# Performance work log

Hardware: AMD Instinct MI355X
Metric: run time of the kernel (lower is better)

## Reference

```python
import jax, jax.numpy as jnp
import numpy as np

MARGIN = 1.0


def setup_inputs() -> dict:
    key = jax.random.key(0)
    k1, k2, k3 = jax.random.split(key, 3)
    N, F = 4096, 512
    a = jax.random.normal(k1, (N, F), dtype=jnp.float32)
    b = jax.random.normal(k2, (N, F), dtype=jnp.float32)
    labels = jax.random.randint(k3, (N,), 0, 16, dtype=jnp.int32)
    return {"a": a, "b": b, "labels": labels}


def reference(a, b, labels):
    # D[i, j] = ||b_i - a_j||  (torch: Xa=a[None], Xb=b[:,None], sum over feat)
    # GEMM form of the pairwise sqdist; clamp tiny fp negatives before sqrt.
    Dsq = (jnp.sum(b * b, axis=1)[:, None]
           + jnp.sum(a * a, axis=1)[None, :]
           - 2.0 * (b @ a.T))
    D = jnp.sqrt(jnp.maximum(Dsq, 0.0))            # [N, N]
    Dexpm = jnp.exp(MARGIN - D)                    # [N, N]

    same = labels[:, None] == labels[None, :]      # [N, N]
    eye = jnp.eye(labels.shape[0], dtype=bool)
    pos_mask = same & ~eye                         # ordered positive pairs (i, j)
    neg_mask = ~same                               # negative pairs (labels differ)

    # neg_i sum for row i: sum_k Dexpm[i, k] over k with labels[k] != labels[i]
    row_negsum = jnp.sum(jnp.where(neg_mask, Dexpm, 0.0), axis=1)  # [N]

    # J_ij = log(neg_ik_sum + neg_jl_sum) + D[i, j]; hinged and squared
    J = jnp.log(row_negsum[:, None] + row_negsum[None, :]) + D
    hinge_sq = jnp.square(jnp.maximum(J, 0.0))

    num_pos = jnp.sum(pos_mask)
    return jnp.sum(jnp.where(pos_mask, hinge_sq, 0.0)) / (2.0 * num_pos)
```

## Files before the change

kernel.cpp:

```cpp
#include <hip/hip_runtime.h>
#include <math.h>

#define NROW 4096
#define FDIM 512
#define MARGIN 1.0f

typedef __attribute__((ext_vector_type(8))) short short8;
typedef __attribute__((ext_vector_type(4))) float floatx4;

__device__ inline unsigned short f2bf(float x) {
    unsigned u = __float_as_uint(x);
    return (unsigned short)((u + 0x7FFFu + ((u >> 16) & 1u)) >> 16);
}
__device__ inline float h2f(unsigned short u) {
    _Float16 h; __builtin_memcpy(&h, &u, 2); return (float)h;
}
__device__ inline unsigned short f2h(float f) {
    _Float16 h = (_Float16)f; unsigned short u; __builtin_memcpy(&u, &h, 2); return u;
}

__global__ __launch_bounds__(64) void prep_kernel(
    const float* __restrict__ a, const float* __restrict__ b,
    unsigned short* __restrict__ abf, unsigned short* __restrict__ bbf,
    float* __restrict__ na, float* __restrict__ nb,
    float* __restrict__ rns, float* __restrict__ loss) {
    int row  = blockIdx.x;
    int lane = threadIdx.x;
    const float4* a4 = (const float4*)(a + (size_t)row * FDIM);
    const float4* b4 = (const float4*)(b + (size_t)row * FDIM);
    ushort4* au = (ushort4*)(abf + (size_t)row * FDIM);
    ushort4* bu = (ushort4*)(bbf + (size_t)row * FDIM);
    float sa = 0.f, sb = 0.f;
    #pragma unroll
    for (int f = lane; f < FDIM / 4; f += 64) {
        float4 va = a4[f];
        float4 vb = b4[f];
        sa += va.x * va.x + va.y * va.y + va.z * va.z + va.w * va.w;
        sb += vb.x * vb.x + vb.y * vb.y + vb.z * vb.z + vb.w * vb.w;
        ushort4 ua = { f2bf(va.x), f2bf(va.y), f2bf(va.z), f2bf(va.w) };
        ushort4 ub = { f2bf(vb.x), f2bf(vb.y), f2bf(vb.z), f2bf(vb.w) };
        au[f] = ua;
        bu[f] = ub;
    }
    #pragma unroll
    for (int o = 32; o > 0; o >>= 1) {
        sa += __shfl_down(sa, o);
        sb += __shfl_down(sb, o);
    }
    if (lane == 0) {
        na[row] = sa;
        nb[row] = sb;
        rns[row] = 0.f;
        if (row == 0) loss[0] = 0.f;
    }
}

template <int MODE>
__global__ __launch_bounds__(256) void pass_mfma(
    const unsigned short* __restrict__ abf, const unsigned short* __restrict__ bbf,
    const int* __restrict__ labels,
    const float* __restrict__ na, const float* __restrict__ nb,
    float* __restrict__ rns, unsigned short* __restrict__ Dws,
    float* __restrict__ loss_sum)
{
    __shared__ __align__(16) unsigned short smem[17408];
    unsigned short* As0 = smem;
    unsigned short* As1 = smem + 4096;
    unsigned short* Bs0 = smem + 8192;
    unsigned short* Bs1 = smem + 12288;
    __shared__ int   li_s[128], lj_s[128];
    __shared__ float nb_s[128], na_s[128], rbi_s[128], rbj_s[128];

    const int t    = threadIdx.x;
    const int lane = t & 63;
    const int w    = t >> 6;
    const int wi   = w >> 1, wj = w & 1;
    const int bid  = blockIdx.x;
    const int sup  = bid >> 6, loc = bid & 63;
    const int by   = ((sup >> 2) << 3) | (loc >> 3);
    const int bx   = ((sup & 3) << 3) | (loc & 7);
    const int ti   = by * 128;
    const int tj   = bx * 128;
    const int lr   = lane & 15;
    const int lq   = lane >> 4;

    floatx4 acc[4][4];
    #pragma unroll
    for (int i = 0; i < 4; ++i)
        #pragma unroll
        for (int j = 0; j < 4; ++j)
            acc[i][j] = (floatx4){0.f, 0.f, 0.f, 0.f};

    if (t < 128) {
        li_s[t] = labels[ti + t];
        nb_s[t] = nb[ti + t];
        if (MODE == 2) rbi_s[t] = rns[ti + t];
    } else {
        int u = t - 128;
        lj_s[u] = labels[tj + u];
        na_s[u] = na[tj + u];
        if (MODE == 2) rbj_s[u] = rns[tj + u];
    }

    for (int kk = 0; kk < FDIM; kk += 64) {
        #pragma unroll
        for (int l = 0; l < 2; ++l) {
            int c   = t + l * 256;
            int row = c >> 2;
            int q   = c & 3;
            size_t ga = (size_t)(tj + row) * FDIM + kk + q * 8;
            size_t gb = (size_t)(ti + row) * FDIM + kk + q * 8;
            __builtin_amdgcn_global_load_lds(
                (const __attribute__((address_space(1))) unsigned int*)(abf + ga),
                (__attribute__((address_space(3))) unsigned int*)(As0 + c * 8), 16, 0, 0);
            __builtin_amdgcn_global_load_lds(
                (const __attribute__((address_space(1))) unsigned int*)(abf + ga + 32),
                (__attribute__((address_space(3))) unsigned int*)(As1 + c * 8), 16, 0, 0);
            __builtin_amdgcn_global_load_lds(
                (const __attribute__((address_space(1))) unsigned int*)(bbf + gb),
                (__attribute__((address_space(3))) unsigned int*)(Bs0 + c * 8), 16, 0, 0);
            __builtin_amdgcn_global_load_lds(
                (const __attribute__((address_space(1))) unsigned int*)(bbf + gb + 32),
                (__attribute__((address_space(3))) unsigned int*)(Bs1 + c * 8), 16, 0, 0);
        }
        __syncthreads();

        {
            short8 af[4], bf[4];
            #pragma unroll
            for (int ri = 0; ri < 4; ++ri)
                af[ri] = *(const short8*)&Bs0[(wi * 64 + ri * 16 + lr) * 32 + lq * 8];
            #pragma unroll
            for (int rj = 0; rj < 4; ++rj)
                bf[rj] = *(const short8*)&As0[(wj * 64 + rj * 16 + lr) * 32 + lq * 8];
            #pragma unroll
            for (int ri = 0; ri < 4; ++ri)
                #pragma unroll
                for (int rj = 0; rj < 4; ++rj)
                    acc[ri][rj] = __builtin_amdgcn_mfma_f32_16x16x32_bf16(
                        af[ri], bf[rj], acc[ri][rj], 0, 0, 0);
        }
        {
            short8 af[4], bf[4];
            #pragma unroll
            for (int ri = 0; ri < 4; ++ri)
                af[ri] = *(const short8*)&Bs1[(wi * 64 + ri * 16 + lr) * 32 + lq * 8];
            #pragma unroll
            for (int rj = 0; rj < 4; ++rj)
                bf[rj] = *(const short8*)&As1[(wj * 64 + rj * 16 + lr) * 32 + lq * 8];
            #pragma unroll
            for (int ri = 0; ri < 4; ++ri)
                #pragma unroll
                for (int rj = 0; rj < 4; ++rj)
                    acc[ri][rj] = __builtin_amdgcn_mfma_f32_16x16x32_bf16(
                        af[ri], bf[rj], acc[ri][rj], 0, 0, 0);
        }
        __syncthreads();
    }

    if (MODE == 0 || MODE == 1) {
        unsigned short* D_s = smem;
        #pragma unroll
        for (int ri = 0; ri < 4; ++ri) {
            float rs[4] = {0.f, 0.f, 0.f, 0.f};
            #pragma unroll
            for (int rj = 0; rj < 4; ++rj) {
                int   jl  = wj * 64 + rj * 16 + lr;
                float naj = na_s[jl];
                int   ljv = lj_s[jl];
                #pragma unroll
                for (int r = 0; r < 4; ++r) {
                    int   il  = wi * 64 + ri * 16 + lq * 4 + r;
                    float dsq = nb_s[il] + naj - 2.f * acc[ri][rj][r];
                    float D   = sqrtf(fmaxf(dsq, 0.f));
                    if (li_s[il] != ljv) rs[r] += __expf(MARGIN - D);
                    if (MODE == 0) D_s[il * 136 + jl] = f2h(D);
                }
            }
            #pragma unroll
            for (int r = 0; r < 4; ++r) {
                #pragma unroll
                for (int o = 8; o > 0; o >>= 1) rs[r] += __shfl_down(rs[r], o, 16);
            }
            if (lr == 0) {
                #pragma unroll
                for (int r = 0; r < 4; ++r)
                    atomicAdd(&rns[ti + wi * 64 + ri * 16 + lq * 4 + r], rs[r]);
            }
        }
        if (MODE == 0) {
            __syncthreads();
            #pragma unroll
            for (int l = 0; l < 8; ++l) {
                int c  = t + l * 256;
                int r  = c >> 4;
                int cw = c & 15;
                *(short8*)&Dws[(size_t)(ti + r) * NROW + tj + cw * 8] =
                    *(const short8*)&D_s[r * 136 + cw * 8];
            }
        }
    } else {
        float local = 0.f;
        #pragma unroll
        for (int ri = 0; ri < 4; ++ri)
            #pragma unroll
            for (int rj = 0; rj < 4; ++rj) {
                int jl  = wj * 64 + rj * 16 + lr;
                int ljv = lj_s[jl];
                float naj = na_s[jl], rbj = rbj_s[jl];
                #pragma unroll
                for (int r = 0; r < 4; ++r) {
                    int il = wi * 64 + ri * 16 + lq * 4 + r;
                    int i  = ti + il, j = tj + jl;
                    if (li_s[il] == ljv && i != j) {
                        float dsq = nb_s[il] + naj - 2.f * acc[ri][rj][r];
                        float D   = sqrtf(fmaxf(dsq, 0.f));
                        float J   = __logf(rbi_s[il] + rbj) + D;
                        float h   = fmaxf(J, 0.f);
                        local += h * h;
                    }
                }
            }
        #pragma unroll
        for (int o = 32; o > 0; o >>= 1) local += __shfl_down(local, o);
        __shared__ float part[4];
        if (lane == 0) part[w] = local;
        __syncthreads();
        if (t == 0) atomicAdd(loss_sum, part[0] + part[1] + part[2] + part[3]);
    }
}

__global__ __launch_bounds__(256) void pass2_sweep(
    const unsigned short* __restrict__ Dws, const int* __restrict__ labels,
    const float* __restrict__ rns, float* __restrict__ loss_sum)
{
    const int t = threadIdx.x;
    float local = 0.f;
    #pragma unroll
    for (int l = 0; l < 4; ++l) {
        int c  = blockIdx.x * 256 + t + l * 524288;
        int i  = c >> 9;
        int j0 = (c & 511) * 8;
        int   li  = labels[i];
        float rbi = rns[i];
        short8 d8 = *(const short8*)&Dws[(size_t)i * NROW + j0];
        int4   la = *(const int4*)&labels[j0];
        int4   lb = *(const int4*)&labels[j0 + 4];
        float4 ra = *(const float4*)&rns[j0];
        float4 rb = *(const float4*)&rns[j0 + 4];
        int   labs[8] = {la.x, la.y, la.z, la.w, lb.x, lb.y, lb.z, lb.w};
        float rnsj[8] = {ra.x, ra.y, ra.z, ra.w, rb.x, rb.y, rb.z, rb.w};
        #pragma unroll
        for (int e = 0; e < 8; ++e) {
            int j = j0 + e;
            if (labs[e] == li && j != i) {
                float J = __logf(rbi + rnsj[e]) + h2f((unsigned short)d8[e]);
                float h = fmaxf(J, 0.f);
                local += h * h;
            }
        }
    }
    #pragma unroll
    for (int o = 32; o > 0; o >>= 1) local += __shfl_down(local, o);
    __shared__ float part[4];
    if ((t & 63) == 0) part[t >> 6] = local;
    __syncthreads();
    if (t == 0) atomicAdd(loss_sum, part[0] + part[1] + part[2] + part[3]);
}

__global__ __launch_bounds__(256) void finalize_kernel(const int* __restrict__ labels,
                                                       const float* __restrict__ loss_sum,
                                                       float* __restrict__ out) {
    __shared__ int hist[16];
    int t = threadIdx.x;
    if (t < 16) hist[t] = 0;
    __syncthreads();
    for (int i = t; i < NROW; i += 256) atomicAdd(&hist[labels[i] & 15], 1);
    __syncthreads();
    if (t == 0) {
        long long np = 0;
        for (int c = 0; c < 16; ++c) np += (long long)hist[c] * (long long)(hist[c] - 1);
        out[0] = loss_sum[0] / (2.0f * (float)np);
    }
}

extern "C" void kernel_launch(void* const* d_in, const int* in_sizes, int n_in,
                              void* d_out, int out_size, void* d_ws, size_t ws_size,
                              hipStream_t stream) {
    const float* a      = (const float*)d_in[0];
    const float* b      = (const float*)d_in[1];
    const int*   labels = (const int*)d_in[2];
    float* out = (float*)d_out;

    unsigned short* abf = (unsigned short*)d_ws;
    unsigned short* bbf = abf + (size_t)NROW * FDIM;
    float* fws  = (float*)(bbf + (size_t)NROW * FDIM);
    float* na   = fws;
    float* nb   = fws + NROW;
    float* rns  = fws + 2 * NROW;
    float* loss = fws + 3 * NROW;
    unsigned short* Dws = (unsigned short*)(fws + 3 * NROW + 4);

    size_t need = ((char*)Dws - (char*)d_ws) + (size_t)NROW * NROW * 2;

    prep_kernel<<<NROW, 64, 0, stream>>>(a, b, abf, bbf, na, nb, rns, loss);

    dim3 grid((NROW / 128) * (NROW / 128));
    if (ws_size >= need) {
        pass_mfma<0><<<grid, 256, 0, stream>>>(abf, bbf, labels, na, nb, rns, Dws, loss);
        pass2_sweep<<<2048, 256, 0, stream>>>(Dws, labels, rns, loss);
    } else {
        pass_mfma<1><<<grid, 256, 0, stream>>>(abf, bbf, labels, na, nb, rns, Dws, loss);
        pass_mfma<2><<<grid, 256, 0, stream>>>(abf, bbf, labels, na, nb, rns, Dws, loss);
    }

    finalize_kernel<<<1, 256, 0, stream>>>(labels, loss, out);
}
```

Measured before the change: 145.8 us.

## Double-buffer K-loop staging to overlap global-to-LDS loads with MFMA

```diff
diff --git a/kernel.cpp b/kernel.cpp
--- a/kernel.cpp
+++ b/kernel.cpp
@@ -63,11 +63,7 @@
     float* __restrict__ rns, unsigned short* __restrict__ Dws,
     float* __restrict__ loss_sum)
 {
-    __shared__ __align__(16) unsigned short smem[17408];
-    unsigned short* As0 = smem;
-    unsigned short* As1 = smem + 4096;
-    unsigned short* Bs0 = smem + 8192;
-    unsigned short* Bs1 = smem + 12288;
+    __shared__ __align__(16) unsigned short arena[17408];
     __shared__ int   li_s[128], lj_s[128];
     __shared__ float nb_s[128], na_s[128], rbi_s[128], rbj_s[128];
 
@@ -102,7 +98,9 @@
         if (MODE == 2) rbj_s[u] = rns[tj + u];
     }
 
-    for (int kk = 0; kk < FDIM; kk += 64) {
+    auto stage = [&](int kk, int buf) {
+        unsigned short* As = arena + buf * 8192;
+        unsigned short* Bs = arena + 4096 + buf * 8192;
         #pragma unroll
         for (int l = 0; l < 2; ++l) {
             int c   = t + l * 256;
@@ -112,54 +110,41 @@
             size_t gb = (size_t)(ti + row) * FDIM + kk + q * 8;
             __builtin_amdgcn_global_load_lds(
                 (const __attribute__((address_space(1))) unsigned int*)(abf + ga),
-                (__attribute__((address_space(3))) unsigned int*)(As0 + c * 8), 16, 0, 0);
-            __builtin_amdgcn_global_load_lds(
-                (const __attribute__((address_space(1))) unsigned int*)(abf + ga + 32),
-                (__attribute__((address_space(3))) unsigned int*)(As1 + c * 8), 16, 0, 0);
+                (__attribute__((address_space(3))) unsigned int*)(As + c * 8), 16, 0, 0);
             __builtin_amdgcn_global_load_lds(
                 (const __attribute__((address_space(1))) unsigned int*)(bbf + gb),
-                (__attribute__((address_space(3))) unsigned int*)(Bs0 + c * 8), 16, 0, 0);
-            __builtin_amdgcn_global_load_lds(
-                (const __attribute__((address_space(1))) unsigned int*)(bbf + gb + 32),
-                (__attribute__((address_space(3))) unsigned int*)(Bs1 + c * 8), 16, 0, 0);
+                (__attribute__((address_space(3))) unsigned int*)(Bs + c * 8), 16, 0, 0);
         }
+    };
+
+    stage(0, 0);
+    __syncthreads();
+
+    #pragma unroll
+    for (int it = 0; it < FDIM / 32; ++it) {
+        if (it < FDIM / 32 - 1) stage((it + 1) * 32, (it + 1) & 1);
+
+        const unsigned short* As = arena + (it & 1) * 8192;
+        const unsigned short* Bs = arena + 4096 + (it & 1) * 8192;
+        short8 af[4], bf[4];
+        #pragma unroll
+        for (int ri = 0; ri < 4; ++ri)
+            af[ri] = *(const short8*)&Bs[(wi * 64 + ri * 16 + lr) * 32 + lq * 8];
+        #pragma unroll
+        for (int rj = 0; rj < 4; ++rj)
+            bf[rj] = *(const short8*)&As[(wj * 64 + rj * 16 + lr) * 32 + lq * 8];
+        #pragma unroll
+        for (int ri = 0; ri < 4; ++ri)
+            #pragma unroll
+            for (int rj = 0; rj < 4; ++rj)
+                acc[ri][rj] = __builtin_amdgcn_mfma_f32_16x16x32_bf16(
+                    af[ri], bf[rj], acc[ri][rj], 0, 0, 0);
+
         __syncthreads();
-
-        {
-            short8 af[4], bf[4];
-            #pragma unroll
-            for (int ri = 0; ri < 4; ++ri)
-                af[ri] = *(const short8*)&Bs0[(wi * 64 + ri * 16 + lr) * 32 + lq * 8];
-            #pragma unroll
-            for (int rj = 0; rj < 4; ++rj)
-                bf[rj] = *(const short8*)&As0[(wj * 64 + rj * 16 + lr) * 32 + lq * 8];
-            #pragma unroll
-            for (int ri = 0; ri < 4; ++ri)
-                #pragma unroll
-                for (int rj = 0; rj < 4; ++rj)
-                    acc[ri][rj] = __builtin_amdgcn_mfma_f32_16x16x32_bf16(
-                        af[ri], bf[rj], acc[ri][rj], 0, 0, 0);
-        }
-        {
-            short8 af[4], bf[4];
-            #pragma unroll
-            for (int ri = 0; ri < 4; ++ri)
-                af[ri] = *(const short8*)&Bs1[(wi * 64 + ri * 16 + lr) * 32 + lq * 8];
-            #pragma unroll
-            for (int rj = 0; rj < 4; ++rj)
-                bf[rj] = *(const short8*)&As1[(wj * 64 + rj * 16 + lr) * 32 + lq * 8];
-            #pragma unroll
-            for (int ri = 0; ri < 4; ++ri)
-                #pragma unroll
-                for (int rj = 0; rj < 4; ++rj)
-                    acc[ri][rj] = __builtin_amdgcn_mfma_f32_16x16x32_bf16(
-                        af[ri], bf[rj], acc[ri][rj], 0, 0, 0);
-        }
-        __syncthreads();
     }
 
     if (MODE == 0 || MODE == 1) {
-        unsigned short* D_s = smem;
+        unsigned short* D_s = arena;
         #pragma unroll
         for (int ri = 0; ri < 4; ++ri) {
             float rs[4] = {0.f, 0.f, 0.f, 0.f};
```

New measurement: 146.1 us. About the same (+0.2%).
